# Performance work log

Measured on AMD Instinct MI355X. Metric: run time of the kernel, lower is better.

Reference implementation:

```python
import jax, jax.numpy as jnp
import numpy as np

MAX_NODE = 511  # config.max_node; padded length = MAX_NODE + 1 (slot 0 = image embedding)


def setup_inputs() -> dict:
    key = jax.random.key(0)
    k1, k2, k3, k4 = jax.random.split(key, 4)
    total_nodes, C, B = 16384, 1024, 32
    return {
        "patch_embeddings": jax.random.normal(k1, (total_nodes, C), dtype=jnp.float32),
        "centroids": jax.random.uniform(k2, (total_nodes, 2), dtype=jnp.float32),
        "image_embedding": jax.random.normal(k3, (B, C), dtype=jnp.float32),
        "num_nodes": jax.random.randint(k4, (B,), 0, 512, dtype=jnp.int32),
    }


def reference(patch_embeddings, centroids, image_embedding, num_nodes):
    # patch_embeddings: [total_nodes, C] flat ragged node features (graphs concatenated)
    # num_nodes: [B] node count per graph; offsets = exclusive cumsum (the torch `cursor`)
    B, C = image_embedding.shape
    offsets = jnp.concatenate([jnp.zeros((1,), jnp.int32),
                               jnp.cumsum(num_nodes)[:-1].astype(jnp.int32)])  # [B]
    j = jnp.arange(MAX_NODE, dtype=jnp.int32)                 # node slot within graph
    n_eff = jnp.minimum(num_nodes, MAX_NODE)                  # truncate oversized graphs
    valid = j[None, :] < n_eff[:, None]                       # [B, MAX_NODE]
    idx = jnp.where(valid, offsets[:, None] + j[None, :], 0)  # safe gather indices

    gathered = patch_embeddings[idx] * valid[..., None]       # [B, MAX_NODE, C]
    features = jnp.concatenate([image_embedding[:, None, :], gathered], axis=1)  # [B, MAX_NODE+1, C]

    cent = centroids[idx] * valid[..., None]                  # [B, MAX_NODE, 2]
    zcol = jnp.zeros((B, 1), jnp.float32)                     # pos 0 for image slot
    pos_x = jnp.concatenate([zcol, cent[..., 0]], axis=1)     # [B, MAX_NODE+1]
    pos_y = jnp.concatenate([zcol, cent[..., 1]], axis=1)

    # torch sets mask[i, n+1:] = True only when n <= max_node (else mask stays all-zero)
    slots = jnp.arange(MAX_NODE + 1)
    mask = ((slots[None, :] >= num_nodes[:, None] + 1)
            & (num_nodes[:, None] <= MAX_NODE)).astype(jnp.float32)

    return features, mask, pos_x, pos_y
```

## Files before the change

kernel.cpp:

```cpp
#include <hip/hip_runtime.h>

#define MAX_NODE 511
#define SLOTS (MAX_NODE + 1)
#define CDIM 1024
#define RPB 4

typedef float f32x4 __attribute__((ext_vector_type(4)));

__global__ __launch_bounds__(256)
void graph_embed_kernel(const float* __restrict__ patch,
                        const float* __restrict__ cent,
                        const float* __restrict__ img,
                        const int*   __restrict__ nn,
                        float* __restrict__ out, int B) {
    const int rb    = blockIdx.x * RPB;
    const int b     = rb >> 9;
    const int slot0 = rb & (SLOTS - 1);
    const int t     = threadIdx.x;
    const int lane  = t & 63;

    int v = (lane < B) ? nn[lane] : 0;
    const int n = __shfl(v, b, 64);
    int c = (lane < b) ? v : 0;
    #pragma unroll
    for (int d = 1; d < 64; d <<= 1) c += __shfl_xor(c, d, 64);
    const int off   = c;
    const int n_eff = (n < MAX_NODE) ? n : MAX_NODE;

    float* features = out;
    float* mask     = out + (size_t)B * SLOTS * CDIM;
    float* pos_x    = mask  + (size_t)B * SLOTS;
    float* pos_y    = pos_x + (size_t)B * SLOTS;

    const f32x4* patch4 = reinterpret_cast<const f32x4*>(patch);
    const f32x4* img4   = reinterpret_cast<const f32x4*>(img);
    f32x4*       feat4  = reinterpret_cast<f32x4*>(features);

    f32x4 r[RPB];
    #pragma unroll
    for (int k = 0; k < RPB; ++k) {
        const int slot = slot0 + k;
        if (slot == 0) {
            r[k] = img4[(size_t)b * (CDIM / 4) + t];
        } else {
            const int j = slot - 1;
            if (j < n_eff) {
                r[k] = patch4[(size_t)(off + j) * (CDIM / 4) + t];
            } else {
                r[k] = (f32x4)(0.f);
            }
        }
    }
    #pragma unroll
    for (int k = 0; k < RPB; ++k) {
        feat4[((size_t)b * SLOTS + slot0 + k) * (CDIM / 4) + t] = r[k];
    }

    if (t < RPB) {
        const int slot = slot0 + t;
        const float m = (slot >= n + 1 && n <= MAX_NODE) ? 1.0f : 0.0f;
        float px = 0.f, py = 0.f;
        if (slot >= 1) {
            const int j = slot - 1;
            if (j < n_eff) {
                px = cent[(size_t)(off + j) * 2 + 0];
                py = cent[(size_t)(off + j) * 2 + 1];
            }
        }
        const size_t mi = (size_t)b * SLOTS + slot;
        mask[mi]  = m;
        pos_x[mi] = px;
        pos_y[mi] = py;
    }
}

extern "C" void kernel_launch(void* const* d_in, const int* in_sizes, int n_in,
                              void* d_out, int out_size, void* d_ws, size_t ws_size,
                              hipStream_t stream) {
    const float* patch = (const float*)d_in[0];
    const float* cent  = (const float*)d_in[1];
    const float* img   = (const float*)d_in[2];
    const int*   nn    = (const int*)d_in[3];
    float* out = (float*)d_out;

    const int B = in_sizes[3];
    const int nblocks = (B * SLOTS) / RPB;
    graph_embed_kernel<<<nblocks, 256, 0, stream>>>(patch, cent, img, nn, out, B);
}
```

Baseline: 19.81 us.

## Switch to grid-strided flat element mapping with shared-memory prefix scan

Replaces the per-block row mapping with a flat grid-stride layout in which each thread handles eight float4 elements spaced a grid apart, and computes the per-graph offsets once per block with a shfl_up scan into shared memory. The aim is to balance work across blocks, hide load latency with more loads in flight per thread, and avoid recomputing the reduction in every wave. The cost is a __syncthreads, per-element index decoding and shared-memory lookups, and mask/pos writes now spread over the first threads of the whole grid.

```diff
diff --git a/kernel.cpp b/kernel.cpp
--- a/kernel.cpp
+++ b/kernel.cpp
@@ -3,29 +3,36 @@
 #define MAX_NODE 511
 #define SLOTS (MAX_NODE + 1)
 #define CDIM 1024
-#define RPB 4
+#define CPR  (CDIM / 4)
+#define ITER 8
+#define THREADS 256
 
 typedef float f32x4 __attribute__((ext_vector_type(4)));
 
-__global__ __launch_bounds__(256)
+__global__ __launch_bounds__(THREADS)
 void graph_embed_kernel(const float* __restrict__ patch,
                         const float* __restrict__ cent,
                         const float* __restrict__ img,
                         const int*   __restrict__ nn,
                         float* __restrict__ out, int B) {
-    const int rb    = blockIdx.x * RPB;
-    const int b     = rb >> 9;
-    const int slot0 = rb & (SLOTS - 1);
-    const int t     = threadIdx.x;
-    const int lane  = t & 63;
+    __shared__ int s_off[64];
+    __shared__ int s_n[64];
 
-    int v = (lane < B) ? nn[lane] : 0;
-    const int n = __shfl(v, b, 64);
-    int c = (lane < b) ? v : 0;
-    #pragma unroll
-    for (int d = 1; d < 64; d <<= 1) c += __shfl_xor(c, d, 64);
-    const int off   = c;
-    const int n_eff = (n < MAX_NODE) ? n : MAX_NODE;
+    const int t    = threadIdx.x;
+    const int lane = t & 63;
+
+    if (t < 64) {
+        int v = (lane < B) ? nn[lane] : 0;
+        int inc = v;
+        #pragma unroll
+        for (int d = 1; d < 64; d <<= 1) {
+            int o = __shfl_up(inc, d, 64);
+            if (lane >= d) inc += o;
+        }
+        s_off[lane] = inc - v;
+        s_n[lane]   = v;
+    }
+    __syncthreads();
 
     float* features = out;
     float* mask     = out + (size_t)B * SLOTS * CDIM;
@@ -36,41 +43,55 @@
     const f32x4* img4   = reinterpret_cast<const f32x4*>(img);
     f32x4*       feat4  = reinterpret_cast<f32x4*>(features);
 
-    f32x4 r[RPB];
+    const size_t total  = (size_t)B * SLOTS * CPR;
+    const size_t g0     = (size_t)blockIdx.x * THREADS + t;
+    const size_t stride = (size_t)gridDim.x * THREADS;
+
+    f32x4 r[ITER];
     #pragma unroll
-    for (int k = 0; k < RPB; ++k) {
-        const int slot = slot0 + k;
-        if (slot == 0) {
-            r[k] = img4[(size_t)b * (CDIM / 4) + t];
-        } else {
-            const int j = slot - 1;
-            if (j < n_eff) {
-                r[k] = patch4[(size_t)(off + j) * (CDIM / 4) + t];
+    for (int i = 0; i < ITER; ++i) {
+        const size_t e = g0 + (size_t)i * stride;
+        if (e < total) {
+            const int row  = (int)(e >> 8);
+            const int col  = (int)(e & (CPR - 1));
+            const int b    = row >> 9;
+            const int slot = row & (SLOTS - 1);
+            const int n    = s_n[b];
+            const int off  = s_off[b];
+            const int n_eff = (n < MAX_NODE) ? n : MAX_NODE;
+            f32x4 v;
+            if (slot == 0) {
+                v = img4[(size_t)b * CPR + col];
+            } else if (slot - 1 < n_eff) {
+                v = patch4[(size_t)(off + slot - 1) * CPR + col];
             } else {
-                r[k] = (f32x4)(0.f);
+                v = (f32x4)(0.f);
             }
+            r[i] = v;
         }
     }
     #pragma unroll
-    for (int k = 0; k < RPB; ++k) {
-        feat4[((size_t)b * SLOTS + slot0 + k) * (CDIM / 4) + t] = r[k];
+    for (int i = 0; i < ITER; ++i) {
+        const size_t e = g0 + (size_t)i * stride;
+        if (e < total) feat4[e] = r[i];
     }
 
-    if (t < RPB) {
-        const int slot = slot0 + t;
+    if (g0 < (size_t)B * SLOTS) {
+        const int row  = (int)g0;
+        const int b    = row >> 9;
+        const int slot = row & (SLOTS - 1);
+        const int n    = s_n[b];
+        const int off  = s_off[b];
+        const int n_eff = (n < MAX_NODE) ? n : MAX_NODE;
         const float m = (slot >= n + 1 && n <= MAX_NODE) ? 1.0f : 0.0f;
         float px = 0.f, py = 0.f;
-        if (slot >= 1) {
-            const int j = slot - 1;
-            if (j < n_eff) {
-                px = cent[(size_t)(off + j) * 2 + 0];
-                py = cent[(size_t)(off + j) * 2 + 1];
-            }
+        if (slot >= 1 && slot - 1 < n_eff) {
+            px = cent[(size_t)(off + slot - 1) * 2 + 0];
+            py = cent[(size_t)(off + slot - 1) * 2 + 1];
         }
-        const size_t mi = (size_t)b * SLOTS + slot;
-        mask[mi]  = m;
-        pos_x[mi] = px;
-        pos_y[mi] = py;
+        mask[g0]  = m;
+        pos_x[g0] = px;
+        pos_y[g0] = py;
     }
 }
 
@@ -84,6 +105,7 @@
     float* out = (float*)d_out;
 
     const int B = in_sizes[3];
-    const int nblocks = (B * SLOTS) / RPB;
-    graph_embed_kernel<<<nblocks, 256, 0, stream>>>(patch, cent, img, nn, out, B);
+    const size_t total = (size_t)B * SLOTS * CPR;
+    const int nblocks = (int)((total + (size_t)THREADS * ITER - 1) / ((size_t)THREADS * ITER));
+    graph_embed_kernel<<<nblocks, THREADS, 0, stream>>>(patch, cent, img, nn, out, B);
 }
```

Measured after the change: 25.91 us. 1.31x slower.
